# Kernel tuning notes

Measured on AMD Instinct MI355X. Metric: run time of the kernel, lower is better.

The kernel has to match this reference:

```python
import jax, jax.numpy as jnp
import numpy as np

B, N, K, C_IN, M, C_OUT = 2, 20000, 16, 128, 9, 128


def setup_inputs() -> dict:
    key = jax.random.key(0)
    k1, k2, k3, k4, k5, k6 = jax.random.split(key, 6)
    x = jax.random.normal(k1, (B, N, C_IN), dtype=jnp.float32)
    # 0 == "no neighbor" (maps to the prepended zero row); valid ids are 1..N
    adj = jax.random.randint(k2, (N, K), 0, N, dtype=jnp.int32)
    W = jax.random.uniform(k3, (M, C_OUT, C_IN), jnp.float32, -0.05, 0.05)
    b = jax.random.uniform(k4, (C_OUT,), jnp.float32, -0.05, 0.05)
    u = jax.random.uniform(k5, (M, C_IN), jnp.float32, -0.05, 0.05)
    c = jax.random.uniform(k6, (M,), jnp.float32, -0.05, 0.05)
    return {"x": x, "adj": adj, "W": W, "b": b, "u": u, "c": c}


def reference(x, adj, W, b, u, c):
    Bb, Nn, Cin = x.shape
    # prepend zero row so adj==0 gathers zeros (padding neighbor)
    xp = jnp.concatenate([jnp.zeros((Bb, 1, Cin), x.dtype), x], axis=1)
    patches = xp[:, adj]                      # [B, N, K, C] neighbor features
    # pseudo-coordinate differences -> soft assignment over M kernels
    diff = x[:, :, None, :] - patches          # [B, N, K, C]
    logits = jnp.einsum('bnkc,mc->bnkm', diff, u) + c
    q = jax.nn.softmax(logits, axis=-1)        # softmax over M (last axis)
    # inverse neighbor count (0 where the node has no neighbors)
    deg = jnp.count_nonzero(adj, axis=1).astype(x.dtype)        # [N]
    deg_inv = jnp.where(deg > 0, 1.0 / jnp.maximum(deg, 1.0), 0.0)
    # out[b,n,o] = deg_inv[n] * sum_{k,m} q[b,n,k,m] * (W[m] @ x_nbr)[o]
    msg = jnp.einsum('bnkm,moc,bnkc->bno', q, W, patches)        # [B, N, O]
    return msg * deg_inv[None, :, None] + b
```

## Files before the change

kernel.cpp:

```cpp
#include <hip/hip_runtime.h>
#include <hip/hip_bf16.h>

#define NB 2
#define NN 20000
#define NKN 16
#define NC 128
#define NM 9
#define NO 128
#define NR (NB*NN)
#define KK (NM*NC)
#define NKC (KK/32)
#define NPB 32
#define YS 12
#define QS (NKN*12+4)
#define YB (NR/64)

typedef short bf16x8 __attribute__((ext_vector_type(8)));
typedef float f32x4 __attribute__((ext_vector_type(4)));
typedef float f32x2 __attribute__((ext_vector_type(2)));
typedef unsigned short u16x8 __attribute__((ext_vector_type(8)));

__device__ inline f32x2 bfpair(unsigned int w) {
    union { unsigned int u; float f; } lo, hi;
    lo.u = w << 16; hi.u = w & 0xFFFF0000u;
    return (f32x2){lo.f, hi.f};
}

__global__ __launch_bounds__(256) void prep_kernel(const float* __restrict__ x,
                                                   const float* __restrict__ u,
                                                   const float* __restrict__ W,
                                                   float* __restrict__ y,
                                                   __hip_bfloat16* __restrict__ xb,
                                                   __hip_bfloat16* __restrict__ Wg,
                                                   int use_xb) {
    int tid = threadIdx.x;
    if (blockIdx.x < YB) {
        int wave = tid >> 6, lane = tid & 63;
        int lr = lane & 15, quad = lane >> 4;
        int node0 = blockIdx.x * 64 + wave * 16;
        long xbase = (long)(node0 + lr) * NC;

        bf16x8 afr[4];
        #pragma unroll
        for (int kc = 0; kc < 4; kc++) {
            const float* px = x + xbase + kc * 32 + quad * 8;
            float4 a0 = *(const float4*)px;
            float4 a1 = *(const float4*)(px + 4);
            union { bf16x8 v; unsigned short s[8]; __hip_bfloat16 h[8]; } af;
            af.h[0] = __float2bfloat16(a0.x); af.h[1] = __float2bfloat16(a0.y);
            af.h[2] = __float2bfloat16(a0.z); af.h[3] = __float2bfloat16(a0.w);
            af.h[4] = __float2bfloat16(a1.x); af.h[5] = __float2bfloat16(a1.y);
            af.h[6] = __float2bfloat16(a1.z); af.h[7] = __float2bfloat16(a1.w);
            afr[kc] = af.v;
            if (use_xb)
                *(u16x8*)((unsigned short*)xb + xbase + kc * 32 + quad * 8) =
                    *(u16x8*)&af.v;
        }
        int cs = (lr < NM) ? lr : 0;
        float fz = (lr < NM) ? 1.f : 0.f;
        f32x4 acc = (f32x4){0.f, 0.f, 0.f, 0.f};
        #pragma unroll
        for (int kc = 0; kc < 4; kc++) {
            const float* pu = u + cs * NC + kc * 32 + quad * 8;
            float4 b0 = *(const float4*)pu;
            float4 b1 = *(const float4*)(pu + 4);
            union { bf16x8 v; __hip_bfloat16 h[8]; } bf;
            bf.h[0] = __float2bfloat16(b0.x * fz); bf.h[1] = __float2bfloat16(b0.y * fz);
            bf.h[2] = __float2bfloat16(b0.z * fz); bf.h[3] = __float2bfloat16(b0.w * fz);
            bf.h[4] = __float2bfloat16(b1.x * fz); bf.h[5] = __float2bfloat16(b1.y * fz);
            bf.h[6] = __float2bfloat16(b1.z * fz); bf.h[7] = __float2bfloat16(b1.w * fz);
            acc = __builtin_amdgcn_mfma_f32_16x16x32_bf16(afr[kc], bf.v, acc, 0, 0, 0);
        }
        if (lr < NM) {
            #pragma unroll
            for (int r = 0; r < 4; r++)
                y[(long)(node0 + quad * 4 + r) * YS + lr] = acc[r];
        }
    } else {
        int t = (blockIdx.x - YB) * 256 + tid;
        int kk = t >> 7;
        int o = t & 127;
        int m = kk >> 7;
        int c = kk & 127;
        float v = W[m * 16384 + o * 128 + c];
        Wg[((kk >> 5) * 128 + o) * 32 + (kk & 31)] = __float2bfloat16(v);
    }
}

template<bool BF16G>
__global__ __launch_bounds__(512, 4) void fused_kernel(const float* __restrict__ x,
                                                       const __hip_bfloat16* __restrict__ xb,
                                                       const int* __restrict__ adj,
                                                       const float* __restrict__ y,
                                                       const float* __restrict__ cv,
                                                       const __hip_bfloat16* __restrict__ Wg,
                                                       const float* __restrict__ bv,
                                                       float* __restrict__ out) {
    __shared__ __align__(16) short s_S[NPB * KK];
    int*   s_adj = (int*)s_S;
    float* s_q   = (float*)((char*)s_S + 2048);

    int tid = threadIdx.x;
    int node0 = blockIdx.x * NPB;
    int b = node0 / NN;
    int n0 = node0 - b * NN;
    int ln = tid >> 4, k = tid & 15;

    int a = adj[(n0 + ln) * NKN + k];
    const float* yn = y + (long)(node0 + ln) * YS;
    const float* ya = y + (long)(b * NN + ((a > 0) ? a - 1 : 0)) * YS;
    float4 yn0 = *(const float4*)yn;
    float4 yn1 = *(const float4*)(yn + 4);
    float  yn8 = yn[8];
    float4 ya0 = *(const float4*)ya;
    float4 ya1 = *(const float4*)(ya + 4);
    float  ya8 = ya[8];
    s_adj[ln * NKN + k] = a;
    __syncthreads();

    int c8 = k << 3;
    int idx[NKN]; int d = 0;
    #pragma unroll
    for (int j = 0; j < NKN; j++) {
        int aa = s_adj[ln * NKN + j];
        d += (aa > 0);
        idx[j] = (aa > 0) ? aa - 1 : 0;
    }
    float di = (d > 0) ? 1.f / (float)d : 0.f;

    uint4 pw0[8];
    if (BF16G) {
        #pragma unroll
        for (int j = 0; j < 8; j++)
            pw0[j] = *(const uint4*)((const unsigned short*)xb +
                                     (long)(b * NN + idx[j]) * NC + c8);
    }

    {
        float sel = (a > 0) ? 1.f : 0.f;
        float l[NM];
        l[0] = yn0.x - sel * ya0.x + cv[0];
        l[1] = yn0.y - sel * ya0.y + cv[1];
        l[2] = yn0.z - sel * ya0.z + cv[2];
        l[3] = yn0.w - sel * ya0.w + cv[3];
        l[4] = yn1.x - sel * ya1.x + cv[4];
        l[5] = yn1.y - sel * ya1.y + cv[5];
        l[6] = yn1.z - sel * ya1.z + cv[6];
        l[7] = yn1.w - sel * ya1.w + cv[7];
        l[8] = yn8   - sel * ya8   + cv[8];
        float mx = l[0];
        #pragma unroll
        for (int m = 1; m < NM; m++) mx = fmaxf(mx, l[m]);
        float e[NM]; float sum = 0.f;
        #pragma unroll
        for (int m = 0; m < NM; m++) { e[m] = expf(l[m] - mx); sum += e[m]; }
        float qs = (a > 0) ? (1.f / sum) : 0.f;
        #pragma unroll
        for (int m = 0; m < NM; m++) s_q[ln * QS + k * 12 + m] = e[m] * qs;
    }
    __syncthreads();

    f32x2 s2[NM][4];
    #pragma unroll
    for (int m = 0; m < NM; m++)
        #pragma unroll
        for (int j = 0; j < 4; j++) s2[m][j] = (f32x2){0.f, 0.f};

    #define ACC_ALL(P0, P1, P2, P3, KK2) {                                    \
        const float* qr = &s_q[ln * QS + (KK2) * 12];                         \
        float4 qa = *(const float4*)qr;                                       \
        float4 qb = *(const float4*)(qr + 4);                                 \
        float  q8 = qr[8];                                                    \
        f32x2 qq;                                                             \
        qq=(f32x2){qa.x,qa.x}; s2[0][0]+=qq*P0; s2[0][1]+=qq*P1; s2[0][2]+=qq*P2; s2[0][3]+=qq*P3; \
        qq=(f32x2){qa.y,qa.y}; s2[1][0]+=qq*P0; s2[1][1]+=qq*P1; s2[1][2]+=qq*P2; s2[1][3]+=qq*P3; \
        qq=(f32x2){qa.z,qa.z}; s2[2][0]+=qq*P0; s2[2][1]+=qq*P1; s2[2][2]+=qq*P2; s2[2][3]+=qq*P3; \
        qq=(f32x2){qa.w,qa.w}; s2[3][0]+=qq*P0; s2[3][1]+=qq*P1; s2[3][2]+=qq*P2; s2[3][3]+=qq*P3; \
        qq=(f32x2){qb.x,qb.x}; s2[4][0]+=qq*P0; s2[4][1]+=qq*P1; s2[4][2]+=qq*P2; s2[4][3]+=qq*P3; \
        qq=(f32x2){qb.y,qb.y}; s2[5][0]+=qq*P0; s2[5][1]+=qq*P1; s2[5][2]+=qq*P2; s2[5][3]+=qq*P3; \
        qq=(f32x2){qb.z,qb.z}; s2[6][0]+=qq*P0; s2[6][1]+=qq*P1; s2[6][2]+=qq*P2; s2[6][3]+=qq*P3; \
        qq=(f32x2){qb.w,qb.w}; s2[7][0]+=qq*P0; s2[7][1]+=qq*P1; s2[7][2]+=qq*P2; s2[7][3]+=qq*P3; \
        qq=(f32x2){q8,q8};     s2[8][0]+=qq*P0; s2[8][1]+=qq*P1; s2[8][2]+=qq*P2; s2[8][3]+=qq*P3; }

    if (BF16G) {
        uint4 pw1[8];
        #pragma unroll
        for (int j = 0; j < 8; j++)
            pw1[j] = *(const uint4*)((const unsigned short*)xb +
                                     (long)(b * NN + idx[8 + j]) * NC + c8);
        #pragma unroll
        for (int j = 0; j < 8; j++) {
            f32x2 p0 = bfpair(pw0[j].x), p1 = bfpair(pw0[j].y);
            f32x2 p2 = bfpair(pw0[j].z), p3 = bfpair(pw0[j].w);
            ACC_ALL(p0, p1, p2, p3, j)
        }
        #pragma unroll
        for (int j = 0; j < 8; j++) {
            f32x2 p0 = bfpair(pw1[j].x), p1 = bfpair(pw1[j].y);
            f32x2 p2 = bfpair(pw1[j].z), p3 = bfpair(pw1[j].w);
            ACC_ALL(p0, p1, p2, p3, 8 + j)
        }
    } else {
        #pragma unroll
        for (int g = 0; g < NKN / 4; g++) {
            float4 fa[4], fb[4];
            #pragma unroll
            for (int j = 0; j < 4; j++) {
                const float* px = x + (long)(b * NN + idx[g * 4 + j]) * NC + c8;
                fa[j] = *(const float4*)px;
                fb[j] = *(const float4*)(px + 4);
            }
            #pragma unroll
            for (int j = 0; j < 4; j++) {
                f32x2 p0 = (f32x2){fa[j].x, fa[j].y}, p1 = (f32x2){fa[j].z, fa[j].w};
                f32x2 p2 = (f32x2){fb[j].x, fb[j].y}, p3 = (f32x2){fb[j].z, fb[j].w};
                ACC_ALL(p0, p1, p2, p3, g * 4 + j)
            }
        }
    }
    #undef ACC_ALL
    __syncthreads();

    #pragma unroll
    for (int m = 0; m < NM; m++) {
        u16x8 ov;
        #pragma unroll
        for (int j = 0; j < 4; j++) {
            union { unsigned short h; __hip_bfloat16 bb; } c0, c1;
            c0.bb = __float2bfloat16(s2[m][j][0] * di);
            c1.bb = __float2bfloat16(s2[m][j][1] * di);
            ov[j * 2]     = c0.h;
            ov[j * 2 + 1] = c1.h;
        }
        int g = m * 16 + k;
        int gs = g ^ (ln & 7);
        *(u16x8*)(&s_S[ln * KK + gs * 8]) = ov;
    }
    __syncthreads();

    int wave = tid >> 6;
    int lane = tid & 63;
    int lr = lane & 15;
    int quad = lane >> 4;
    const short* wg = reinterpret_cast<const short*>(Wg);
    f32x4 acc0 = (f32x4){0.f, 0.f, 0.f, 0.f};
    f32x4 acc1 = (f32x4){0.f, 0.f, 0.f, 0.f};

    #pragma unroll 9
    for (int kc = 0; kc < NKC; kc++) {
        int g = kc * 4 + quad;
        int gs = g ^ (lr & 7);
        bf16x8 bfrag = *(const bf16x8*)(wg + ((kc * 128) + wave * 16 + lr) * 32 + quad * 8);
        bf16x8 a0 = *(const bf16x8*)(&s_S[lr * KK + gs * 8]);
        bf16x8 a1 = *(const bf16x8*)(&s_S[(16 + lr) * KK + gs * 8]);
        acc0 = __builtin_amdgcn_mfma_f32_16x16x32_bf16(a0, bfrag, acc0, 0, 0, 0);
        acc1 = __builtin_amdgcn_mfma_f32_16x16x32_bf16(a1, bfrag, acc1, 0, 0, 0);
    }

    int col = wave * 16 + lr;
    float bb = bv[col];
    int rbase = node0 + quad * 4;
    #pragma unroll
    for (int r = 0; r < 4; r++) {
        out[(long)(rbase + r) * NO + col]      = acc0[r] + bb;
        out[(long)(rbase + 16 + r) * NO + col] = acc1[r] + bb;
    }
}

extern "C" void kernel_launch(void* const* d_in, const int* in_sizes, int n_in,
                              void* d_out, int out_size, void* d_ws, size_t ws_size,
                              hipStream_t stream) {
    const float* x   = (const float*)d_in[0];
    const int*   adj = (const int*)  d_in[1];
    const float* W   = (const float*)d_in[2];
    const float* bv  = (const float*)d_in[3];
    const float* u   = (const float*)d_in[4];
    const float* cv  = (const float*)d_in[5];
    float* out = (float*)d_out;

    char* ws = (char*)d_ws;
    float* y = (float*)ws;
    __hip_bfloat16* Wg = (__hip_bfloat16*)(ws + 1920000);
    __hip_bfloat16* xb = (__hip_bfloat16*)(ws + 2214912);
    bool use_xb = (ws_size >= (size_t)12454912);

    prep_kernel<<<YB + 576, 256, 0, stream>>>(x, u, W, y, use_xb ? xb : nullptr, Wg,
                                              use_xb ? 1 : 0);
    if (use_xb)
        fused_kernel<true><<<NR / NPB, 512, 0, stream>>>(x, xb, adj, y, cv, Wg, bv, out);
    else
        fused_kernel<false><<<NR / NPB, 512, 0, stream>>>(x, xb, adj, y, cv, Wg, bv, out);
}
```

Baseline: 135.5 us.

## Compute per-node q-weighted neighbor aggregation with MFMA via transposed LDS reads

Replaces the scalar FMA accumulation of q times neighbor features with a per-node MFMA. Each thread stages one whole neighbor row (bf16) plus split hi/lo bf16 q values in LDS, and ds_read_b64_tr_b16 loads the transposed fragments. Degree is now computed with a wave ballot/popcount instead of an LDS adjacency pass, and W is re-laid out in a channel-tile-major K order to match the new S layout. It uses a much larger shared allocation (160KB), which drops occupancy to 2 blocks per SM, and adds extra precision handling for q through the hi/lo split.

```diff
diff --git a/kernel.cpp b/kernel.cpp
--- a/kernel.cpp
+++ b/kernel.cpp
@@ -9,21 +9,22 @@
 #define NO 128
 #define NR (NB*NN)
 #define KK (NM*NC)
-#define NKC (KK/32)
 #define NPB 32
 #define YS 12
-#define QS (NKN*12+4)
 #define YB (NR/64)
+#define QTOFF 131072u
 
 typedef short bf16x8 __attribute__((ext_vector_type(8)));
-typedef float f32x4 __attribute__((ext_vector_type(4)));
-typedef float f32x2 __attribute__((ext_vector_type(2)));
+typedef short bf16x4 __attribute__((ext_vector_type(4)));
+typedef float f32x4  __attribute__((ext_vector_type(4)));
 typedef unsigned short u16x8 __attribute__((ext_vector_type(8)));
 
-__device__ inline f32x2 bfpair(unsigned int w) {
-    union { unsigned int u; float f; } lo, hi;
-    lo.u = w << 16; hi.u = w & 0xFFFF0000u;
-    return (f32x2){lo.f, hi.f};
+union frg8 { bf16x4 h[2]; bf16x8 v; };
+
+__device__ inline unsigned short bfb(float f) {
+    union { __hip_bfloat16 b; unsigned short u; } t;
+    t.b = __float2bfloat16(f);
+    return t.u;
 }
 
 __global__ __launch_bounds__(256) void prep_kernel(const float* __restrict__ x,
@@ -80,15 +81,17 @@
         int t = (blockIdx.x - YB) * 256 + tid;
         int kk = t >> 7;
         int o = t & 127;
-        int m = kk >> 7;
-        int c = kk & 127;
-        float v = W[m * 16384 + o * 128 + c];
+        int ctt = kk / 144;
+        int rem = kk - ctt * 144;
+        int m = rem >> 4;
+        int ci = rem & 15;
+        float v = W[m * 16384 + o * 128 + ctt * 16 + ci];
         Wg[((kk >> 5) * 128 + o) * 32 + (kk & 31)] = __float2bfloat16(v);
     }
 }
 
 template<bool BF16G>
-__global__ __launch_bounds__(512, 4) void fused_kernel(const float* __restrict__ x,
+__global__ __launch_bounds__(512, 2) void fused_kernel(const float* __restrict__ x,
                                                        const __hip_bfloat16* __restrict__ xb,
                                                        const int* __restrict__ adj,
                                                        const float* __restrict__ y,
@@ -96,168 +99,156 @@
                                                        const __hip_bfloat16* __restrict__ Wg,
                                                        const float* __restrict__ bv,
                                                        float* __restrict__ out) {
-    __shared__ __align__(16) short s_S[NPB * KK];
-    int*   s_adj = (int*)s_S;
-    float* s_q   = (float*)((char*)s_S + 2048);
+    __shared__ __align__(16) char smem[163840];
 
     int tid = threadIdx.x;
     int node0 = blockIdx.x * NPB;
     int b = node0 / NN;
     int n0 = node0 - b * NN;
     int ln = tid >> 4, k = tid & 15;
+    int lane = tid & 63, wv = tid >> 6;
+    int lr = lane & 15, quad = lane >> 4;
 
     int a = adj[(n0 + ln) * NKN + k];
+    long row = (long)(b * NN + ((a > 0) ? a - 1 : 0));
+
     const float* yn = y + (long)(node0 + ln) * YS;
-    const float* ya = y + (long)(b * NN + ((a > 0) ? a - 1 : 0)) * YS;
+    const float* ya = y + row * YS;
     float4 yn0 = *(const float4*)yn;
     float4 yn1 = *(const float4*)(yn + 4);
     float  yn8 = yn[8];
     float4 ya0 = *(const float4*)ya;
     float4 ya1 = *(const float4*)(ya + 4);
     float  ya8 = ya[8];
-    s_adj[ln * NKN + k] = a;
+
+    uint4 pw[16];
+    if (BF16G) {
+        const uint4* xr = (const uint4*)(xb + row * NC);
+        #pragma unroll
+        for (int i = 0; i < 16; i++) pw[i] = xr[i];
+    }
+
+    unsigned long long mk = __ballot(a > 0);
+    int d = (int)__popcll((mk >> (quad * 16)) & 0xFFFFull);
+    float di = (d > 0) ? 1.f / (float)d : 0.f;
+
+    float sel = (a > 0) ? 1.f : 0.f;
+    float l[NM];
+    l[0] = yn0.x - sel * ya0.x + cv[0];
+    l[1] = yn0.y - sel * ya0.y + cv[1];
+    l[2] = yn0.z - sel * ya0.z + cv[2];
+    l[3] = yn0.w - sel * ya0.w + cv[3];
+    l[4] = yn1.x - sel * ya1.x + cv[4];
+    l[5] = yn1.y - sel * ya1.y + cv[5];
+    l[6] = yn1.z - sel * ya1.z + cv[6];
+    l[7] = yn1.w - sel * ya1.w + cv[7];
+    l[8] = yn8   - sel * ya8   + cv[8];
+    float mx = l[0];
+    #pragma unroll
+    for (int m = 1; m < NM; m++) mx = fmaxf(mx, l[m]);
+    float e_[NM]; float sum = 0.f;
+    #pragma unroll
+    for (int m = 0; m < NM; m++) { e_[m] = expf(l[m] - mx); sum += e_[m]; }
+    float qf = ((a > 0) ? (1.f / sum) : 0.f) * di;
+
+    union { u16x8 v[2]; unsigned short s[16]; } H, L;
+    #pragma unroll
+    for (int m = 0; m < NM; m++) {
+        float qv = e_[m] * qf;
+        unsigned short hb = bfb(qv);
+        union { unsigned short u; __hip_bfloat16 bb; } hh; hh.u = hb;
+        float hf = __bfloat162float(hh.bb);
+        H.s[m] = hb;
+        L.s[m] = bfb(qv - hf);
+    }
+    #pragma unroll
+    for (int m = NM; m < 16; m++) { H.s[m] = 0; L.s[m] = 0; }
+
+    unsigned qo = QTOFF + (unsigned)(ln * 1024 + (k >> 2) * 128 + (k & 3) * 32);
+    *(u16x8*)(smem + qo)        = H.v[0];
+    *(u16x8*)(smem + qo + 16)   = H.v[1];
+    *(u16x8*)(smem + qo + 512)  = L.v[0];
+    *(u16x8*)(smem + qo + 528)  = L.v[1];
+
+    unsigned po = (unsigned)(ln * 4096 + (k >> 2) * 128 + (k & 3) * 32);
+    if (BF16G) {
+        #pragma unroll
+        for (int i = 0; i < 16; i++)
+            *(uint4*)(smem + po + (i >> 1) * 512 + (i & 1) * 16) = pw[i];
+    } else {
+        const float4* xf = (const float4*)(x + row * NC);
+        #pragma unroll
+        for (int i = 0; i < 16; i++) {
+            float4 fa = xf[2 * i], fb2 = xf[2 * i + 1];
+            union { u16x8 v; unsigned short s[8]; } o;
+            o.s[0] = bfb(fa.x);  o.s[1] = bfb(fa.y);
+            o.s[2] = bfb(fa.z);  o.s[3] = bfb(fa.w);
+            o.s[4] = bfb(fb2.x); o.s[5] = bfb(fb2.y);
+            o.s[6] = bfb(fb2.z); o.s[7] = bfb(fb2.w);
+            *(u16x8*)(smem + po + (i >> 1) * 512 + (i & 1) * 16) = o.v;
+        }
+    }
+
+    asm volatile("s_waitcnt lgkmcnt(0)" ::: "memory");
+    __builtin_amdgcn_sched_barrier(0);
+
+    unsigned sb = (unsigned)(unsigned long long)(uintptr_t)&smem[0];
+
+    #pragma unroll
+    for (int g = 0; g < 4; ++g) {
+        int n = (wv << 2) + g;
+        bf16x4 qa0, qa1;
+        unsigned qaddr = sb + QTOFF + (unsigned)(n * 1024 + quad * 256 + lr * 8);
+        asm volatile("ds_read_b64_tr_b16 %0, %2 offset:0\n\t"
+                     "ds_read_b64_tr_b16 %1, %2 offset:128"
+                     : "=&v"(qa0), "=&v"(qa1) : "v"(qaddr));
+        bf16x4 pb0[8], pb1[8];
+        unsigned paddr = sb + (unsigned)(n * 4096 + (quad & 1) * 256 + lr * 8);
+        #pragma unroll
+        for (int t = 0; t < 8; ++t)
+            asm volatile("ds_read_b64_tr_b16 %0, %2 offset:%c3\n\t"
+                         "ds_read_b64_tr_b16 %1, %2 offset:%c4"
+                         : "=&v"(pb0[t]), "=&v"(pb1[t])
+                         : "v"(paddr), "i"(t * 512), "i"(t * 512 + 128));
+        asm volatile("s_waitcnt lgkmcnt(0)" ::: "memory");
+        __builtin_amdgcn_sched_barrier(0);
+
+        frg8 af; af.h[0] = qa0; af.h[1] = qa1;
+        unsigned swz = (unsigned)((n & 7) << 4);
+        unsigned sbase = (unsigned)(n * 4096);
+        #pragma unroll
+        for (int t = 0; t < 8; ++t) {
+            frg8 bf_; bf_.h[0] = pb0[t]; bf_.h[1] = pb1[t];
+            f32x4 acc = (f32x4){0.f, 0.f, 0.f, 0.f};
+            acc = __builtin_amdgcn_mfma_f32_16x16x32_bf16(af.v, bf_.v, acc, 0, 0, 0);
+            #pragma unroll
+            for (int r = 0; r < 4; ++r) {
+                int m = quad * 4 + r;
+                if (m < 9) {
+                    unsigned off = ((unsigned)(t * 288 + m * 32 + lr * 2)) ^ swz;
+                    *(short*)(smem + sbase + off) = (short)bfb(acc[r]);
+                }
+            }
+        }
+    }
+
     __syncthreads();
 
-    int c8 = k << 3;
-    int idx[NKN]; int d = 0;
-    #pragma unroll
-    for (int j = 0; j < NKN; j++) {
-        int aa = s_adj[ln * NKN + j];
-        d += (aa > 0);
-        idx[j] = (aa > 0) ? aa - 1 : 0;
-    }
-    float di = (d > 0) ? 1.f / (float)d : 0.f;
-
-    uint4 pw0[8];
-    if (BF16G) {
-        #pragma unroll
-        for (int j = 0; j < 8; j++)
-            pw0[j] = *(const uint4*)((const unsigned short*)xb +
-                                     (long)(b * NN + idx[j]) * NC + c8);
-    }
-
-    {
-        float sel = (a > 0) ? 1.f : 0.f;
-        float l[NM];
-        l[0] = yn0.x - sel * ya0.x + cv[0];
-        l[1] = yn0.y - sel * ya0.y + cv[1];
-        l[2] = yn0.z - sel * ya0.z + cv[2];
-        l[3] = yn0.w - sel * ya0.w + cv[3];
-        l[4] = yn1.x - sel * ya1.x + cv[4];
-        l[5] = yn1.y - sel * ya1.y + cv[5];
-        l[6] = yn1.z - sel * ya1.z + cv[6];
-        l[7] = yn1.w - sel * ya1.w + cv[7];
-        l[8] = yn8   - sel * ya8   + cv[8];
-        float mx = l[0];
-        #pragma unroll
-        for (int m = 1; m < NM; m++) mx = fmaxf(mx, l[m]);
-        float e[NM]; float sum = 0.f;
-        #pragma unroll
-        for (int m = 0; m < NM; m++) { e[m] = expf(l[m] - mx); sum += e[m]; }
-        float qs = (a > 0) ? (1.f / sum) : 0.f;
-        #pragma unroll
-        for (int m = 0; m < NM; m++) s_q[ln * QS + k * 12 + m] = e[m] * qs;
-    }
-    __syncthreads();
-
-    f32x2 s2[NM][4];
-    #pragma unroll
-    for (int m = 0; m < NM; m++)
-        #pragma unroll
-        for (int j = 0; j < 4; j++) s2[m][j] = (f32x2){0.f, 0.f};
-
-    #define ACC_ALL(P0, P1, P2, P3, KK2) {                                    \
-        const float* qr = &s_q[ln * QS + (KK2) * 12];                         \
-        float4 qa = *(const float4*)qr;                                       \
-        float4 qb = *(const float4*)(qr + 4);                                 \
-        float  q8 = qr[8];                                                    \
-        f32x2 qq;                                                             \
-        qq=(f32x2){qa.x,qa.x}; s2[0][0]+=qq*P0; s2[0][1]+=qq*P1; s2[0][2]+=qq*P2; s2[0][3]+=qq*P3; \
-        qq=(f32x2){qa.y,qa.y}; s2[1][0]+=qq*P0; s2[1][1]+=qq*P1; s2[1][2]+=qq*P2; s2[1][3]+=qq*P3; \
-        qq=(f32x2){qa.z,qa.z}; s2[2][0]+=qq*P0; s2[2][1]+=qq*P1; s2[2][2]+=qq*P2; s2[2][3]+=qq*P3; \
-        qq=(f32x2){qa.w,qa.w}; s2[3][0]+=qq*P0; s2[3][1]+=qq*P1; s2[3][2]+=qq*P2; s2[3][3]+=qq*P3; \
-        qq=(f32x2){qb.x,qb.x}; s2[4][0]+=qq*P0; s2[4][1]+=qq*P1; s2[4][2]+=qq*P2; s2[4][3]+=qq*P3; \
-        qq=(f32x2){qb.y,qb.y}; s2[5][0]+=qq*P0; s2[5][1]+=qq*P1; s2[5][2]+=qq*P2; s2[5][3]+=qq*P3; \
-        qq=(f32x2){qb.z,qb.z}; s2[6][0]+=qq*P0; s2[6][1]+=qq*P1; s2[6][2]+=qq*P2; s2[6][3]+=qq*P3; \
-        qq=(f32x2){qb.w,qb.w}; s2[7][0]+=qq*P0; s2[7][1]+=qq*P1; s2[7][2]+=qq*P2; s2[7][3]+=qq*P3; \
-        qq=(f32x2){q8,q8};     s2[8][0]+=qq*P0; s2[8][1]+=qq*P1; s2[8][2]+=qq*P2; s2[8][3]+=qq*P3; }
-
-    if (BF16G) {
-        uint4 pw1[8];
-        #pragma unroll
-        for (int j = 0; j < 8; j++)
-            pw1[j] = *(const uint4*)((const unsigned short*)xb +
-                                     (long)(b * NN + idx[8 + j]) * NC + c8);
-        #pragma unroll
-        for (int j = 0; j < 8; j++) {
-            f32x2 p0 = bfpair(pw0[j].x), p1 = bfpair(pw0[j].y);
-            f32x2 p2 = bfpair(pw0[j].z), p3 = bfpair(pw0[j].w);
-            ACC_ALL(p0, p1, p2, p3, j)
-        }
-        #pragma unroll
-        for (int j = 0; j < 8; j++) {
-            f32x2 p0 = bfpair(pw1[j].x), p1 = bfpair(pw1[j].y);
-            f32x2 p2 = bfpair(pw1[j].z), p3 = bfpair(pw1[j].w);
-            ACC_ALL(p0, p1, p2, p3, 8 + j)
-        }
-    } else {
-        #pragma unroll
-        for (int g = 0; g < NKN / 4; g++) {
-            float4 fa[4], fb[4];
-            #pragma unroll
-            for (int j = 0; j < 4; j++) {
-                const float* px = x + (long)(b * NN + idx[g * 4 + j]) * NC + c8;
-                fa[j] = *(const float4*)px;
-                fb[j] = *(const float4*)(px + 4);
-            }
-            #pragma unroll
-            for (int j = 0; j < 4; j++) {
-                f32x2 p0 = (f32x2){fa[j].x, fa[j].y}, p1 = (f32x2){fa[j].z, fa[j].w};
-                f32x2 p2 = (f32x2){fb[j].x, fb[j].y}, p3 = (f32x2){fb[j].z, fb[j].w};
-                ACC_ALL(p0, p1, p2, p3, g * 4 + j)
-            }
-        }
-    }
-    #undef ACC_ALL
-    __syncthreads();
-
-    #pragma unroll
-    for (int m = 0; m < NM; m++) {
-        u16x8 ov;
-        #pragma unroll
-        for (int j = 0; j < 4; j++) {
-            union { unsigned short h; __hip_bfloat16 bb; } c0, c1;
-            c0.bb = __float2bfloat16(s2[m][j][0] * di);
-            c1.bb = __float2bfloat16(s2[m][j][1] * di);
-            ov[j * 2]     = c0.h;
-            ov[j * 2 + 1] = c1.h;
-        }
-        int g = m * 16 + k;
-        int gs = g ^ (ln & 7);
-        *(u16x8*)(&s_S[ln * KK + gs * 8]) = ov;
-    }
-    __syncthreads();
-
-    int wave = tid >> 6;
-    int lane = tid & 63;
-    int lr = lane & 15;
-    int quad = lane >> 4;
     const short* wg = reinterpret_cast<const short*>(Wg);
     f32x4 acc0 = (f32x4){0.f, 0.f, 0.f, 0.f};
     f32x4 acc1 = (f32x4){0.f, 0.f, 0.f, 0.f};
-
+    unsigned swzB = (unsigned)((lr & 7) << 4);
     #pragma unroll 9
-    for (int kc = 0; kc < NKC; kc++) {
-        int g = kc * 4 + quad;
-        int gs = g ^ (lr & 7);
-        bf16x8 bfrag = *(const bf16x8*)(wg + ((kc * 128) + wave * 16 + lr) * 32 + quad * 8);
-        bf16x8 a0 = *(const bf16x8*)(&s_S[lr * KK + gs * 8]);
-        bf16x8 a1 = *(const bf16x8*)(&s_S[(16 + lr) * KK + gs * 8]);
+    for (int kc = 0; kc < 36; kc++) {
+        bf16x8 bfrag = *(const bf16x8*)(wg + ((kc * 128) + wv * 16 + lr) * 32 + quad * 8);
+        unsigned ao = ((unsigned)(kc * 64 + quad * 16)) ^ swzB;
+        bf16x8 a0 = *(const bf16x8*)(smem + (unsigned)(lr * 4096) + ao);
+        bf16x8 a1 = *(const bf16x8*)(smem + (unsigned)((16 + lr) * 4096) + ao);
         acc0 = __builtin_amdgcn_mfma_f32_16x16x32_bf16(a0, bfrag, acc0, 0, 0, 0);
         acc1 = __builtin_amdgcn_mfma_f32_16x16x32_bf16(a1, bfrag, acc1, 0, 0, 0);
     }
 
-    int col = wave * 16 + lr;
+    int col = wv * 16 + lr;
     float bb = bv[col];
     int rbase = node0 + quad * 4;
     #pragma unroll
```

New measurement: 161.5 us. 19.2% more time.
